# Kernel tuning notes

Hardware: AMD Instinct MI355X
Metric: run time of the kernel (lower is better)

The kernel has to match this reference:

```python
import jax, jax.numpy as jnp
import numpy as np

K = 1.0          # manifold curvature parameter (Lorentz hyperboloid <x,x>_L = -K)
NUM_HEADS = 16
LN_EPS = 1e-5
MID_EPS = 1e-8


def add_time(space):
    # lift a space-like vector onto the hyperboloid: x0 = sqrt(||s||^2 + K)
    t = jnp.sqrt(jnp.sum(space * space, axis=-1, keepdims=True) + K)
    return jnp.concatenate([t, space], axis=-1)


def hlinear(x, W, b):
    # Lorentz linear: dense map on full ambient vector -> space part, recompute time
    return add_time(jnp.einsum('...d,od->...o', x, W) + b)


def hyp_layernorm(x, g, b):
    s = x[..., 1:]
    mu = jnp.mean(s, axis=-1, keepdims=True)
    var = jnp.mean((s - mu) ** 2, axis=-1, keepdims=True)
    s = (s - mu) * jax.lax.rsqrt(var + LN_EPS) * g + b
    return add_time(s)


def hyp_relu(x):
    return add_time(jax.nn.relu(x[..., 1:]))


def lorentz_norm(v):
    # sqrt(|<v,v>_L|) with clamp for numerical safety
    inner = -v[..., 0] ** 2 + jnp.sum(v[..., 1:] ** 2, axis=-1)
    return jnp.sqrt(jnp.maximum(jnp.abs(inner), MID_EPS))


def midpoint_pair(z, x):
    # manifold.midpoint(stack([z, x], dim=-2)).squeeze(): mean then project back
    ave = 0.5 * (z + x)
    return jnp.sqrt(K) * ave / lorentz_norm(ave)[..., None]


def attention(x, Wq, bq, Wk, bk, Wv, bv, Wo, bo):
    B, S, D = x.shape
    dim = D - 1
    H = NUM_HEADS
    dh = dim // H

    def split_heads(t):
        # drop time, split space into heads, re-lift each head onto hyperboloid
        s = t[..., 1:].reshape(B, S, H, dh).transpose(0, 2, 1, 3)  # [B,H,S,dh]
        return add_time(s)                                          # [B,H,S,dh+1]

    qh = split_heads(hlinear(x, Wq, bq))
    kh = split_heads(hlinear(x, Wk, bk))
    vh = split_heads(hlinear(x, Wv, bv))

    # pairwise Lorentz inner product; scores = -d_L^2 / sqrt(dh)
    inner = (jnp.einsum('bhid,bhjd->bhij', qh[..., 1:], kh[..., 1:])
             - qh[..., 0][..., :, None] * kh[..., 0][..., None, :])
    scores = (2.0 / K + 2.0 * inner) / jnp.sqrt(jnp.asarray(dh, x.dtype))
    att = jax.nn.softmax(scores, axis=-1)

    # Lorentz midpoint aggregation of values (weights sum to 1)
    ave = jnp.einsum('bhij,bhjd->bhid', att, vh)
    out = jnp.sqrt(K) * ave / lorentz_norm(ave)[..., None]  # [B,H,S,dh+1]

    # concat head space parts, re-lift, output projection
    out_space = out[..., 1:].transpose(0, 2, 1, 3).reshape(B, S, dim)
    return hlinear(add_time(out_space), Wo, bo)


def reference(x, Wq, bq, Wk, bk, Wv, bv, Wo, bo, ln1_g, ln1_b, W1, c1, W2, c2, ln2_g, ln2_b):
    z = attention(x, Wq, bq, Wk, bk, Wv, bv, Wo, bo)
    x = midpoint_pair(z, x)
    x = hyp_layernorm(x, ln1_g, ln1_b)
    h = hyp_relu(hlinear(x, W1, c1))
    z = hlinear(h, W2, c2)
    x = midpoint_pair(z, x)
    x = hyp_layernorm(x, ln2_g, ln2_b)
    return x


def setup_inputs() -> dict:
    key = jax.random.key(0)
    ks = jax.random.split(key, 12)
    B, S, dim, mlp = 4, 1024, 1024, 4096
    D = dim + 1
    sc = 0.02
    x = add_time(jax.random.normal(ks[0], (B, S, dim), dtype=jnp.float32))
    return {
        'x': x,
        'Wq': sc * jax.random.normal(ks[1], (dim, D), dtype=jnp.float32),
        'bq': jnp.zeros((dim,), jnp.float32),
        'Wk': sc * jax.random.normal(ks[2], (dim, D), dtype=jnp.float32),
        'bk': jnp.zeros((dim,), jnp.float32),
        'Wv': sc * jax.random.normal(ks[3], (dim, D), dtype=jnp.float32),
        'bv': jnp.zeros((dim,), jnp.float32),
        'Wo': sc * jax.random.normal(ks[4], (dim, D), dtype=jnp.float32),
        'bo': jnp.zeros((dim,), jnp.float32),
        'ln1_g': jnp.ones((dim,), jnp.float32),
        'ln1_b': jnp.zeros((dim,), jnp.float32),
        'W1': sc * jax.random.normal(ks[5], (mlp, D), dtype=jnp.float32),
        'c1': jnp.zeros((mlp,), jnp.float32),
        'W2': sc * jax.random.normal(ks[6], (dim, mlp + 1), dtype=jnp.float32),
        'c2': jnp.zeros((dim,), jnp.float32),
        'ln2_g': jnp.ones((dim,), jnp.float32),
        'ln2_b': jnp.zeros((dim,), jnp.float32),
    }
```

## Files before the change

### kernel.cpp

```cpp
#include <hip/hip_runtime.h>

typedef unsigned short u16;
typedef unsigned int   u32;
typedef short bf16x8 __attribute__((ext_vector_type(8)));
typedef float f32x4  __attribute__((ext_vector_type(4)));

#define NTOK 4096
#define SEQ  1024

#define BARRIER() __builtin_amdgcn_s_barrier()
#define VMCNT(n) asm volatile("s_waitcnt vmcnt(" #n ")" ::: "memory")

__device__ __forceinline__ u16 f2bf(float f){
  union { float f; u32 u; } x; x.f = f;
  u32 r = (x.u + 0x7FFFu + ((x.u >> 16) & 1u)) >> 16;
  return (u16)r;
}
__device__ __forceinline__ float bf2f(u16 u){
  union { u32 u; float f; } x; x.u = ((u32)u) << 16; return x.f;
}
__device__ __forceinline__ void gl_lds16(const void* gp, void* lp){
  __builtin_amdgcn_global_load_lds(
      (const __attribute__((address_space(1))) u32*)gp,
      (__attribute__((address_space(3))) u32*)lp, 16, 0, 0);
}

__global__ __launch_bounds__(256) void conv_x(const float* __restrict__ x,
                                              u16* __restrict__ xs, float* __restrict__ xt){
  int t = blockIdx.x * 256 + threadIdx.x;
  int tok = t >> 10, i = t & 1023;
  xs[t] = f2bf(x[(size_t)tok * 1025 + 1 + i]);
  if (i == 0) xt[tok] = x[(size_t)tok * 1025];
}

__global__ __launch_bounds__(256) void conv_w_all(
    const float* __restrict__ Wq, const float* __restrict__ Wk,
    const float* __restrict__ Wv, const float* __restrict__ Wo,
    const float* __restrict__ W1, const float* __restrict__ W2,
    u16* __restrict__ wqkv, u16* __restrict__ wo_s, u16* __restrict__ w1_s, u16* __restrict__ w2_s,
    float* __restrict__ wqkv0, float* __restrict__ wo0, float* __restrict__ w10, float* __restrict__ w20)
{
  int t = blockIdx.x * 256 + threadIdx.x;
  const int M1 = 1 << 20;
  const float* W; u16* Wb; float* w0; int shift; int idx;
  if (t < 4 * M1){
    int region = t >> 20; idx = t & (M1 - 1); shift = 10;
    if (region == 0)      { W = Wq; Wb = wqkv;          w0 = wqkv0; }
    else if (region == 1) { W = Wk; Wb = wqkv + M1;     w0 = wqkv0 + 1024; }
    else if (region == 2) { W = Wv; Wb = wqkv + 2 * M1; w0 = wqkv0 + 2048; }
    else                  { W = Wo; Wb = wo_s;          w0 = wo0; }
  } else if (t < 8 * M1){
    idx = t - 4 * M1; shift = 10; W = W1; Wb = w1_s; w0 = w10;
  } else {
    idx = t - 8 * M1; shift = 12; W = W2; Wb = w2_s; w0 = w20;
  }
  int Kin = 1 << shift;
  int r = idx >> shift, i = idx & (Kin - 1);
  Wb[idx] = f2bf(W[(size_t)r * (Kin + 1) + 1 + i]);
  if (i == 0) w0[r] = W[(size_t)r * (Kin + 1)];
}

__global__ __launch_bounds__(256) void v_transpose(const u16* __restrict__ qkv,
                                                   const float* __restrict__ vtm,
                                                   u16* __restrict__ vT){
  __shared__ u16 tile[64 * 72];
  const int tid = threadIdx.x;
  const int kt = blockIdx.x, bh = blockIdx.y;
  const int b = bh >> 4, h = bh & 15;
  #pragma unroll
  for (int i = 0; i < 2; i++){
    int c = tid * 2 + i;
    int key = c >> 3, fc = c & 7;
    uint4 v = *(const uint4*)(qkv + ((size_t)(b * 1024 + kt * 64 + key)) * 3072 + 2048 + h * 64 + fc * 8);
    *(uint4*)&tile[key * 72 + fc * 8] = v;
  }
  __syncthreads();
  for (int c = tid; c < 520; c += 256){
    int vtr = c >> 3, kc = c & 7;
    union { uint4 v; u16 s[8]; } d;
    if (vtr == 0){
      #pragma unroll
      for (int j = 0; j < 8; j++) d.s[j] = f2bf(vtm[(size_t)bh * 1024 + kt * 64 + kc * 8 + j]);
    } else {
      int f = vtr - 1;
      #pragma unroll
      for (int j = 0; j < 8; j++) d.s[j] = tile[(kc * 8 + j) * 72 + f];
    }
    *(uint4*)(vT + ((size_t)bh * 65 + vtr) * 1024 + kt * 64 + kc * 8) = d.v;
  }
}

__global__ __launch_bounds__(512, 2) void gemm_bt(
    const u16* __restrict__ Ag, int lda, const u16* __restrict__ Bg, int ldb,
    const float* __restrict__ at, int at_mode, const float* __restrict__ b0,
    const float* __restrict__ bias_a, const float* __restrict__ bias_b, const float* __restrict__ bias_c,
    u16* __restrict__ Cbf, int ldc, int Kslice, int mode,
    float* __restrict__ qtv, float* __restrict__ ktv, float* __restrict__ vtm,
    float* __restrict__ rowsq)
{
  __shared__ u16 smem[65536];
  const int tid = threadIdx.x;
  const int w = tid >> 6, l = tid & 63;
  const int l15 = l & 15, q = l >> 4;
  const int wr = w >> 2, wc = w & 3;
  const int gx = gridDim.x;
  const int nwg = gx * gridDim.y;
  const int lin = blockIdx.y * gx + blockIdx.x;
  const int swz = (lin & 7) * (nwg >> 3) + (lin >> 3);
  const int m0 = (swz / gx) * 256, n0 = (swz % gx) * 256;
  const int ks = blockIdx.z;
  const int kbeg = ks * Kslice;

  f32x4 acc[8][4] = {};
  bf16x8 af[4][2], b0f[2][2], b1f[2][2];

  auto stageA = [&](int kt, int buf, int qm){
    #pragma unroll
    for (int ii = 0; ii < 2; ii++){
      int s = (w * 2 + ii) * 64 + l;
      int kk = s >> 9, rem = s & 511;
      int ridx = rem >> 2, cp = rem & 3;
      int kc = (cp - (ridx >> 1)) & 3;
      int trow = ((ridx >> 6) << 7) + qm * 64 + (ridx & 63);
      gl_lds16(Ag + (size_t)(m0 + trow) * lda + kt + kk * 32 + kc * 8,
               &smem[(buf * 2 + qm) * 8192 + (w * 2 + ii) * 512]);
    }
  };
  auto stageB = [&](int kt, int buf, int qn){
    #pragma unroll
    for (int ii = 0; ii < 2; ii++){
      int s = (w * 2 + ii) * 64 + l;
      int kk = s >> 9, rem = s & 511;
      int ridx = rem >> 2, cp = rem & 3;
      int kc = (cp - (ridx >> 1)) & 3;
      int trow = ((ridx >> 5) << 6) + qn * 32 + (ridx & 31);
      gl_lds16(Bg + (size_t)(n0 + trow) * ldb + kt + kk * 32 + kc * 8,
               &smem[32768 + (buf * 2 + qn) * 8192 + (w * 2 + ii) * 512]);
    }
  };
  auto loadA = [&](int buf, int qm){
    #pragma unroll
    for (int i2 = 0; i2 < 4; i2++){
      int ridx = wr * 64 + i2 * 16 + l15;
      int slot = ridx * 4 + ((q + (ridx >> 1)) & 3);
      #pragma unroll
      for (int kk = 0; kk < 2; kk++)
        af[i2][kk] = *(const bf16x8*)&smem[(buf * 2 + qm) * 8192 + kk * 4096 + slot * 8];
    }
  };
  auto loadB = [&](int buf, int qn, bf16x8 (&bb)[2][2]){
    #pragma unroll
    for (int j2 = 0; j2 < 2; j2++){
      int ridx = wc * 32 + j2 * 16 + l15;
      int slot = ridx * 4 + ((q + (ridx >> 1)) & 3);
      #pragma unroll
      for (int kk = 0; kk < 2; kk++)
        bb[j2][kk] = *(const bf16x8*)&smem[32768 + (buf * 2 + qn) * 8192 + kk * 4096 + slot * 8];
    }
  };
  auto mma4 = [&](int qm, int qn, bf16x8 (&bb)[2][2]){
    __builtin_amdgcn_s_setprio(1);
    #pragma unroll
    for (int i2 = 0; i2 < 4; i2++)
      #pragma unroll
      for (int j2 = 0; j2 < 2; j2++)
        #pragma unroll
        for (int kk = 0; kk < 2; kk++)
          acc[qm * 4 + i2][qn * 2 + j2] = __builtin_amdgcn_mfma_f32_16x16x32_bf16(
              af[i2][kk], bb[j2][kk], acc[qm * 4 + i2][qn * 2 + j2], 0, 0, 0);
    __builtin_amdgcn_s_setprio(0);
  };

  stageA(kbeg, 0, 0);
  stageB(kbeg, 0, 0);
  stageB(kbeg, 0, 1);
  stageA(kbeg, 0, 1);
  stageA(kbeg + 64, 1, 0);
  stageB(kbeg + 64, 1, 1);
  stageA(kbeg + 64, 1, 1);
  VMCNT(6);
  BARRIER();

  const int NI = Kslice >> 7;
  for (int it = 0; it < NI; it++){
    const int kb = kbeg + it * 128;
    const bool more = (it + 1 < NI);
    loadA(0, 0); loadB(0, 0, b0f);
    stageB(kb + 64, 1, 0);
    BARRIER(); mma4(0, 0, b0f); BARRIER();
    loadB(0, 1, b1f);
    if (more) stageA(kb + 128, 0, 0);
    BARRIER(); mma4(0, 1, b1f); BARRIER();
    loadA(0, 1);
    if (more) stageB(kb + 128, 0, 1);
    BARRIER(); mma4(1, 1, b1f); BARRIER();
    loadB(0, 0, b0f);
    if (more) stageA(kb + 128, 0, 1);
    if (more) { VMCNT(6); } else { VMCNT(0); }
    BARRIER(); mma4(1, 0, b0f); BARRIER();
    loadA(1, 0); loadB(1, 0, b0f);
    if (more) stageB(kb + 128, 0, 0);
    BARRIER(); mma4(0, 0, b0f); BARRIER();
    loadB(1, 1, b1f);
    if (more) stageA(kb + 192, 1, 0);
    BARRIER(); mma4(0, 1, b1f); BARRIER();
    loadA(1, 1);
    if (more) stageB(kb + 192, 1, 1);
    BARRIER(); mma4(1, 1, b1f); BARRIER();
    loadB(1, 0, b0f);
    if (more) stageA(kb + 192, 1, 1);
    if (more) { VMCNT(6); }
    BARRIER(); mma4(1, 0, b0f); BARRIER();
  }

  const size_t Mtot = (size_t)gridDim.y * 256;
  const size_t slice_off = (size_t)ks * Mtot * ldc;
  #pragma unroll
  for (int ai = 0; ai < 8; ai++){
    const int rb = wr * 128 + (ai >> 2) * 64 + (ai & 3) * 16 + q * 4;
    float atv[4];
    #pragma unroll
    for (int r = 0; r < 4; r++){
      float a = at[m0 + rb + r];
      atv[r] = at_mode ? sqrtf(a + 1.f) : a;
    }
    float p[4] = {0.f, 0.f, 0.f, 0.f};
    #pragma unroll
    for (int bj = 0; bj < 4; bj++){
      const int col = n0 + wc * 64 + (bj >> 1) * 32 + (bj & 1) * 16 + l15;
      float b0v = b0[col];
      float bv;
      if (mode == 0) bv = (col < 1024) ? bias_a[col] : (col < 2048) ? bias_b[col - 1024] : bias_c[col - 2048];
      else bv = bias_a[col];
      #pragma unroll
      for (int r = 0; r < 4; r++){
        size_t row = (size_t)(m0 + rb + r);
        float add = (ks == 0) ? (atv[r] * b0v + bv) : 0.f;
        float v = acc[ai][bj][r] + add;
        if (mode == 2) v = fmaxf(v, 0.f);
        Cbf[slice_off + row * ldc + col] = f2bf(v);
        if (mode != 1) p[r] += v * v;
      }
    }
    if (mode != 1){
      #pragma unroll
      for (int r = 0; r < 4; r++){
        float s = p[r];
        s += __shfl_xor(s, 1, 64); s += __shfl_xor(s, 2, 64);
        s += __shfl_xor(s, 4, 64); s += __shfl_xor(s, 8, 64);
        if (l15 == 0){
          int row = m0 + rb + r;
          if (mode == 2){
            atomicAdd(&rowsq[row], s);
          } else {
            int ch = (n0 + wc * 64) >> 6;
            int bb = row >> 10, sidx = row & 1023;
            float t = sqrtf(s + 1.f);
            if (ch < 16)      qtv[((size_t)bb * 16 + ch) * 1024 + sidx] = t;
            else if (ch < 32) ktv[((size_t)bb * 16 + ch - 16) * 1024 + sidx] = t;
            else              vtm[((size_t)bb * 16 + ch - 32) * 1024 + sidx] = t;
          }
        }
      }
    }
  }
}

__global__ __launch_bounds__(512) void attn_kernel(
    const u16* __restrict__ qkv, const float* __restrict__ qt,
    const float* __restrict__ ktm, const u16* __restrict__ vT,
    u16* __restrict__ aout, float* __restrict__ aot_sq)
{
  __shared__ u16 smem[30720];
  u16* Qlds = smem;
  u16* Kl0 = smem + 8192;
  u16* Kl1 = smem + 12288;
  u16* Vl0 = smem + 16384;
  u16* Vl1 = smem;
  u16* Plds = smem + 21504;
  const int tid = threadIdx.x;
  const int w = tid >> 6, l = tid & 63;
  const int l15 = l & 15, qd = l >> 4;
  const int q0 = blockIdx.x * 128;
  const int bh = blockIdx.y;
  const int b = bh >> 4, h = bh & 15;
  const size_t tokbase = (size_t)b << 10;

  #pragma unroll
  for (int i = 0; i < 2; i++){
    int c = i * 512 + w * 64 + l;
    int row = c >> 3, kc = ((c & 7) - row) & 7;
    gl_lds16(qkv + (tokbase + q0 + row) * 3072 + h * 64 + kc * 8, &Qlds[(i * 512 + w * 64) * 8]);
  }
  __syncthreads();
  bf16x8 aq[2];
  {
    int row = w * 16 + l15;
    #pragma unroll
    for (int kk = 0; kk < 2; kk++)
      aq[kk] = *(const bf16x8*)&Qlds[(row * 8 + ((kk * 4 + qd + row) & 7)) * 8];
  }
  float tq[4];
  #pragma unroll
  for (int r = 0; r < 4; r++)
    tq[r] = qt[(size_t)bh * SEQ + q0 + w * 16 + qd * 4 + r];

  auto stage_kv = [&](int kt, int buf){
    u16* K = buf ? Kl1 : Kl0;
    u16* V = buf ? Vl1 : Vl0;
    int c = w * 64 + l;
    int row = c >> 3, kc = ((c & 7) - row) & 7;
    gl_lds16(qkv + (tokbase + kt * 64 + row) * 3072 + 1024 + h * 64 + kc * 8, &K[w * 512]);
    gl_lds16(vT + ((size_t)bh * 65 + row) * 1024 + kt * 64 + kc * 8, &V[w * 512]);
    if (w == 0 && l < 8)
      gl_lds16(vT + ((size_t)bh * 65 + 64) * 1024 + kt * 64 + (l & 7) * 8, &V[4096]);
  };

  float mrow[4] = {-1e30f, -1e30f, -1e30f, -1e30f};
  f32x4 acco[5] = {};

  stage_kv(0, 0);
  for (int kt = 0; kt < 16; kt++){
    __syncthreads();
    if (kt + 1 < 16) stage_kv(kt + 1, (kt + 1) & 1);
    u16* K = (kt & 1) ? Kl1 : Kl0;
    u16* V = (kt & 1) ? Vl1 : Vl0;

    float sc[4][4];
    float mx[4] = {-1e30f, -1e30f, -1e30f, -1e30f};
    #pragma unroll
    for (int ct = 0; ct < 4; ct++){
      f32x4 z = {0.f, 0.f, 0.f, 0.f};
      int key = ct * 16 + l15;
      #pragma unroll
      for (int kk = 0; kk < 2; kk++){
        bf16x8 bk = *(const bf16x8*)&K[(key * 8 + ((kk * 4 + qd + key) & 7)) * 8];
        z = __builtin_amdgcn_mfma_f32_16x16x32_bf16(aq[kk], bk, z, 0, 0, 0);
      }
      float tk = ktm[(size_t)bh * SEQ + kt * 64 + key];
      #pragma unroll
      for (int r = 0; r < 4; r++){
        float s = 0.25f + 0.25f * (z[r] - tq[r] * tk);
        sc[ct][r] = s;
        mx[r] = fmaxf(mx[r], s);
      }
    }
    #pragma unroll
    for (int r = 0; r < 4; r++){
      #pragma unroll
      for (int msk = 1; msk < 16; msk <<= 1)
        mx[r] = fmaxf(mx[r], __shfl_xor(mx[r], msk, 64));
      float mnew = fmaxf(mrow[r], mx[r]);
      float alpha = __expf(mrow[r] - mnew);
      mrow[r] = mnew;
      #pragma unroll
      for (int co = 0; co < 5; co++) acco[co][r] *= alpha;
      mx[r] = mnew;
    }
    #pragma unroll
    for (int ct = 0; ct < 4; ct++)
      #pragma unroll
      for (int r = 0; r < 4; r++)
        Plds[w * 1152 + (qd * 4 + r) * 72 + ct * 16 + l15] = f2bf(__expf(sc[ct][r] - mx[r]));
    asm volatile("s_waitcnt lgkmcnt(0)" ::: "memory");
    bf16x8 ap[2];
    #pragma unroll
    for (int kk = 0; kk < 2; kk++)
      ap[kk] = *(const bf16x8*)&Plds[w * 1152 + l15 * 72 + kk * 32 + qd * 8];
    #pragma unroll
    for (int co = 0; co < 5; co++){
      int vtr = co * 16 + l15;
      #pragma unroll
      for (int kk = 0; kk < 2; kk++){
        bf16x8 bv = *(const bf16x8*)&V[(vtr * 8 + ((kk * 4 + qd + vtr) & 7)) * 8];
        acco[co] = __builtin_amdgcn_mfma_f32_16x16x32_bf16(ap[kk], bv, acco[co], 0, 0, 0);
      }
    }
  }
  #pragma unroll
  for (int r = 0; r < 4; r++){
    float ss = 0.f;
    #pragma unroll
    for (int co = 0; co < 5; co++){
      int col = co * 16 + l15;
      float v = acco[co][r];
      if (col == 0) ss -= v * v;
      else if (col < 65) ss += v * v;
    }
    #pragma unroll
    for (int msk = 1; msk < 16; msk <<= 1) ss += __shfl_xor(ss, msk, 64);
    float v0b = __shfl(acco[0][r], l & 48, 64);
    float sp = ss + v0b * v0b;
    float rn = rsqrtf(fmaxf(fabsf(ss), 1e-8f));
    size_t rowg = tokbase + q0 + w * 16 + qd * 4 + r;
    if (l15 == 0) atomicAdd(&aot_sq[rowg], sp * rn * rn);
    #pragma unroll
    for (int co = 0; co < 5; co++){
      int col = co * 16 + l15;
      if (col >= 1 && col < 65)
        aout[rowg * 1024 + h * 64 + col - 1] = f2bf(acco[co][r] * rn);
    }
  }
}

__device__ __forceinline__ float block_sum(float v, float* red){
  int tid = threadIdx.x;
  #pragma unroll
  for (int m = 1; m < 64; m <<= 1) v += __shfl_xor(v, m, 64);
  __syncthreads();
  if ((tid & 63) == 0) red[tid >> 6] = v;
  __syncthreads();
  return red[0] + red[1] + red[2] + red[3];
}

__global__ __launch_bounds__(256) void mid_ln(
    const u16* __restrict__ z, const u16* __restrict__ xsb, const float* __restrict__ xtv,
    const float* __restrict__ gam, const float* __restrict__ bet,
    u16* __restrict__ ob, float* __restrict__ ot,
    float* __restrict__ ofull, int mode_out, int nsl)
{
  __shared__ float red[4];
  const int tid = threadIdx.x;
  const int tok = blockIdx.x;
  float zv[4], xv[4], xtime;
  xtime = xtv[tok];
  {
    const u16* xr = xsb + (size_t)tok * 1024;
    #pragma unroll
    for (int j = 0; j < 4; j++) xv[j] = bf2f(xr[tid + j * 256]);
  }
  {
    #pragma unroll
    for (int j = 0; j < 4; j++) zv[j] = 0.f;
    for (int s = 0; s < nsl; s++){
      const u16* zs = z + (size_t)s * NTOK * 1024 + (size_t)tok * 1024;
      #pragma unroll
      for (int j = 0; j < 4; j++) zv[j] += bf2f(zs[tid + j * 256]);
    }
  }
  float ssz = 0.f;
  #pragma unroll
  for (int j = 0; j < 4; j++) ssz += zv[j] * zv[j];
  ssz = block_sum(ssz, red);
  float tz = sqrtf(ssz + 1.f);
  float av[4]; float ssa = 0.f;
  #pragma unroll
  for (int j = 0; j < 4; j++){ av[j] = 0.5f * (zv[j] + xv[j]); ssa += av[j] * av[j]; }
  ssa = block_sum(ssa, red);
  float avt = 0.5f * (tz + xtime);
  float rn = rsqrtf(fmaxf(fabsf(ssa - avt * avt), 1e-8f));
  float uv[4]; float su = 0.f, squ = 0.f;
  #pragma unroll
  for (int j = 0; j < 4; j++){ uv[j] = av[j] * rn; su += uv[j]; squ += uv[j] * uv[j]; }
  su = block_sum(su, red);
  squ = block_sum(squ, red);
  float mu = su * (1.f / 1024.f);
  float var = squ * (1.f / 1024.f) - mu * mu;
  float rv = rsqrtf(fmaxf(var, 0.f) + 1e-5f);
  float sv[4]; float sss = 0.f;
  #pragma unroll
  for (int j = 0; j < 4; j++){
    int i = tid + j * 256;
    sv[j] = (uv[j] - mu) * rv * gam[i] + bet[i];
    sss += sv[j] * sv[j];
  }
  sss = block_sum(sss, red);
  float tout = sqrtf(sss + 1.f);
  if (mode_out == 0){
    #pragma unroll
    for (int j = 0; j < 4; j++){
      int i = tid + j * 256;
      ob[(size_t)tok * 1024 + i] = f2bf(sv[j]);
    }
    if (tid == 0) ot[tok] = tout;
  } else {
    float* orow = ofull + (size_t)tok * 1025;
    #pragma unroll
    for (int j = 0; j < 4; j++) orow[1 + tid + j * 256] = sv[j];
    if (tid == 0) orow[0] = tout;
  }
}

extern "C" void kernel_launch(void* const* d_in, const int* in_sizes, int n_in,
                              void* d_out, int out_size, void* d_ws, size_t ws_size,
                              hipStream_t stream){
  const float* x   = (const float*)d_in[0];
  const float* Wq  = (const float*)d_in[1];
  const float* bq  = (const float*)d_in[2];
  const float* Wk  = (const float*)d_in[3];
  const float* bk  = (const float*)d_in[4];
  const float* Wv  = (const float*)d_in[5];
  const float* bv  = (const float*)d_in[6];
  const float* Wo  = (const float*)d_in[7];
  const float* bo  = (const float*)d_in[8];
  const float* g1  = (const float*)d_in[9];
  const float* be1 = (const float*)d_in[10];
  const float* W1  = (const float*)d_in[11];
  const float* c1  = (const float*)d_in[12];
  const float* W2  = (const float*)d_in[13];
  const float* c2  = (const float*)d_in[14];
  const float* g2  = (const float*)d_in[15];
  const float* be2 = (const float*)d_in[16];
  float* out = (float*)d_out;

  char* p = (char*)d_ws;
  auto take = [&](size_t n){ char* r = p; p += (n + 255) & ~(size_t)255; return r; };
  u16*   xs    = (u16*)  take((size_t)NTOK * 1024 * 2);
  float* xt    = (float*)take(NTOK * 4);
  u16*   wqkv  = (u16*)  take((size_t)3072 * 1024 * 2);
  float* wqkv0 = (float*)take(3072 * 4);
  u16*   wo_s  = (u16*)  take((size_t)1024 * 1024 * 2);
  float* wo0   = (float*)take(1024 * 4);
  u16*   w1_s  = (u16*)  take((size_t)4096 * 1024 * 2);
  float* w10   = (float*)take(4096 * 4);
  u16*   w2_s  = (u16*)  take((size_t)1024 * 4096 * 2);
  float* w20   = (float*)take(1024 * 4);
  u16*   qkvb  = (u16*)  take((size_t)NTOK * 3072 * 2);
  float* qtv   = (float*)take((size_t)64 * 1024 * 4);
  float* ktv   = (float*)take((size_t)64 * 1024 * 4);
  float* vtm   = (float*)take((size_t)64 * 1024 * 4);
  u16*   vT    = (u16*)  take((size_t)64 * 65 * 1024 * 2);
  u16*   aoutb = (u16*)  take((size_t)NTOK * 1024 * 2);
  float* sqbuf = (float*)take((size_t)2 * NTOK * 4);
  float* aot_sq = sqbuf;
  float* htv_sq = sqbuf + NTOK;
  u16*   zbuf  = (u16*)  take((size_t)4 * NTOK * 1024 * 2);
  u16*   x1b   = (u16*)  take((size_t)NTOK * 1024 * 2);
  float* x1t   = (float*)take(NTOK * 4);
  u16*   hbuf  = (u16*)  take((size_t)NTOK * 4096 * 2);

  hipMemsetAsync(sqbuf, 0, (size_t)2 * NTOK * 4, stream);

  conv_x<<<NTOK * 1024 / 256, 256, 0, stream>>>(x, xs, xt);
  conv_w_all<<<(12 * 1024 * 1024) / 256, 256, 0, stream>>>(
      Wq, Wk, Wv, Wo, W1, W2, wqkv, wo_s, w1_s, w2_s, wqkv0, wo0, w10, w20);

  gemm_bt<<<dim3(12, 16), 512, 0, stream>>>(xs, 1024, wqkv, 1024, xt, 0, wqkv0,
      bq, bk, bv, qkvb, 3072, 1024, 0, qtv, ktv, vtm, nullptr);
  v_transpose<<<dim3(16, 64), 512 / 2, 0, stream>>>(qkvb, vtm, vT);
  attn_kernel<<<dim3(8, 64), 512, 0, stream>>>(qkvb, qtv, ktv, vT, aoutb, aot_sq);
  gemm_bt<<<dim3(4, 16, 4), 512, 0, stream>>>(aoutb, 1024, wo_s, 1024, aot_sq, 1, wo0,
      bo, nullptr, nullptr, zbuf, 1024, 256, 1, nullptr, nullptr, nullptr, nullptr);
  mid_ln<<<NTOK, 256, 0, stream>>>(zbuf, xs, xt, g1, be1,
      x1b, x1t, nullptr, 0, 4);
  gemm_bt<<<dim3(16, 16), 512, 0, stream>>>(x1b, 1024, w1_s, 1024, x1t, 0, w10,
      c1, nullptr, nullptr, hbuf, 4096, 1024, 2, nullptr, nullptr, nullptr, htv_sq);
  gemm_bt<<<dim3(4, 16, 4), 512, 0, stream>>>(hbuf, 4096, w2_s, 4096, htv_sq, 1, w20,
      c2, nullptr, nullptr, zbuf, 1024, 1024, 1, nullptr, nullptr, nullptr, nullptr);
  mid_ln<<<NTOK, 256, 0, stream>>>(zbuf, x1b, x1t, g2, be2,
      nullptr, nullptr, out, 1, 4);
}
```

Baseline: 413.7 us.

## Add 128x128 GEMM kernel for QKV/out/W2 projections and raise MFMA priority in attention

Introduces a new 256-thread GEMM kernel with 128x128 tiles and double-buffered LDS staging. The QKV, output-projection and W2 GEMMs now use it, with more blocks and split-K reduced from 4 to 2, which halves the partial sums mid_ln has to combine. The 256-tile kernel is kept only for W1 and has its epilogue trimmed. The attention kernel wraps its MFMA sections in s_setprio so matrix work gets issued first. The aim is better CU occupancy and load balance on the narrower GEMMs, at the cost of less data reuse per tile.

```diff
diff --git a/kernel.cpp b/kernel.cpp
--- a/kernel.cpp
+++ b/kernel.cpp
@@ -90,12 +90,128 @@
   }
 }
 
-__global__ __launch_bounds__(512, 2) void gemm_bt(
-    const u16* __restrict__ Ag, int lda, const u16* __restrict__ Bg, int ldb,
+__global__ __launch_bounds__(256) void gemm128(
+    const u16* __restrict__ A, int lda, const u16* __restrict__ Bm, int ldb,
     const float* __restrict__ at, int at_mode, const float* __restrict__ b0,
     const float* __restrict__ bias_a, const float* __restrict__ bias_b, const float* __restrict__ bias_c,
     u16* __restrict__ Cbf, int ldc, int Kslice, int mode,
     float* __restrict__ qtv, float* __restrict__ ktv, float* __restrict__ vtm,
+    float* __restrict__ rowsq)
+{
+  __shared__ u16 As[2][128 * 64];
+  __shared__ u16 Bs[2][128 * 64];
+  const int tid = threadIdx.x;
+  const int w = tid >> 6, l = tid & 63;
+  const int l15 = l & 15, q = l >> 4;
+  const int m0 = blockIdx.y * 128, n0 = blockIdx.x * 128;
+  const int ks = blockIdx.z;
+  const int kbeg = ks * Kslice;
+  const int kend = kbeg + Kslice;
+  const int wr = w >> 1, wc = w & 1;
+  f32x4 acc[4][4] = {};
+
+  auto stage = [&](int kt, int buf){
+    #pragma unroll
+    for (int half = 0; half < 2; half++){
+      #pragma unroll
+      for (int i = 0; i < 2; i++){
+        int s = (w * 2 + i) * 64 + l;
+        int row = s >> 2;
+        int kc = ((s & 3) - (s >> 3)) & 3;
+        gl_lds16(A  + (size_t)(m0 + row) * lda + kt + half * 32 + kc * 8,
+                 &As[buf][half * 4096 + (w * 2 + i) * 512]);
+        gl_lds16(Bm + (size_t)(n0 + row) * ldb + kt + half * 32 + kc * 8,
+                 &Bs[buf][half * 4096 + (w * 2 + i) * 512]);
+      }
+    }
+  };
+  auto compute = [&](int buf, int half){
+    bf16x8 af[4], bfr[4];
+    #pragma unroll
+    for (int i = 0; i < 4; i++){
+      int row = wr * 64 + i * 16 + l15;
+      int slot = row * 4 + ((q + (row >> 1)) & 3);
+      af[i] = *(const bf16x8*)&As[buf][half * 4096 + slot * 8];
+    }
+    #pragma unroll
+    for (int j = 0; j < 4; j++){
+      int row = wc * 64 + j * 16 + l15;
+      int slot = row * 4 + ((q + (row >> 1)) & 3);
+      bfr[j] = *(const bf16x8*)&Bs[buf][half * 4096 + slot * 8];
+    }
+    #pragma unroll
+    for (int i = 0; i < 4; i++)
+      #pragma unroll
+      for (int j = 0; j < 4; j++)
+        acc[i][j] = __builtin_amdgcn_mfma_f32_16x16x32_bf16(af[i], bfr[j], acc[i][j], 0, 0, 0);
+  };
+
+  stage(kbeg, 0);
+  for (int kt = kbeg; kt < kend; kt += 128){
+    __syncthreads();
+    if (kt + 64 < kend) stage(kt + 64, 1);
+    compute(0, 0); compute(0, 1);
+    __syncthreads();
+    if (kt + 128 < kend) stage(kt + 128, 0);
+    compute(1, 0); compute(1, 1);
+  }
+
+  const size_t slice_off = (size_t)ks * (size_t)(gridDim.y * 128) * ldc;
+  #pragma unroll
+  for (int i = 0; i < 4; i++){
+    float atv[4];
+    #pragma unroll
+    for (int r = 0; r < 4; r++){
+      float a = at[m0 + wr * 64 + i * 16 + q * 4 + r];
+      atv[r] = at_mode ? sqrtf(a + 1.f) : a;
+    }
+    float p[4] = {0.f, 0.f, 0.f, 0.f};
+    #pragma unroll
+    for (int j = 0; j < 4; j++){
+      int col = n0 + wc * 64 + j * 16 + l15;
+      float b0v = b0[col];
+      float bv;
+      if (mode == 0) bv = (col < 1024) ? bias_a[col] : (col < 2048) ? bias_b[col - 1024] : bias_c[col - 2048];
+      else bv = bias_a[col];
+      #pragma unroll
+      for (int r = 0; r < 4; r++){
+        size_t row = (size_t)(m0 + wr * 64 + i * 16 + q * 4 + r);
+        float add = (ks == 0) ? (atv[r] * b0v + bv) : 0.f;
+        float v = acc[i][j][r] + add;
+        if (mode == 2) v = fmaxf(v, 0.f);
+        Cbf[slice_off + row * ldc + col] = f2bf(v);
+        if (mode != 1) p[r] += v * v;
+      }
+    }
+    if (mode != 1){
+      #pragma unroll
+      for (int r = 0; r < 4; r++){
+        float s = p[r];
+        s += __shfl_xor(s, 1, 64); s += __shfl_xor(s, 2, 64);
+        s += __shfl_xor(s, 4, 64); s += __shfl_xor(s, 8, 64);
+        if (l15 == 0){
+          int row = m0 + wr * 64 + i * 16 + q * 4 + r;
+          if (mode == 2){
+            atomicAdd(&rowsq[row], s);
+          } else {
+            int ch = (n0 + wc * 64) >> 6;
+            int bb = row >> 10, sidx = row & 1023;
+            float t = sqrtf(s + 1.f);
+            if (ch < 16)      qtv[((size_t)bb * 16 + ch) * 1024 + sidx] = t;
+            else if (ch < 32) ktv[((size_t)bb * 16 + ch - 16) * 1024 + sidx] = t;
+            else              vtm[((size_t)bb * 16 + ch - 32) * 1024 + sidx] = t;
+          }
+        }
+      }
+    }
+  }
+}
+
+__global__ __launch_bounds__(512, 2) void gemm256(
+    const u16* __restrict__ Ag, int lda, const u16* __restrict__ Bg, int ldb,
+    const float* __restrict__ at, int at_mode, const float* __restrict__ b0,
+    const float* __restrict__ bias_a,
+    u16* __restrict__ Cbf, int ldc, int Kslice, int mode,
     float* __restrict__ rowsq)
 {
   __shared__ u16 smem[65536];
@@ -229,9 +345,7 @@
     for (int bj = 0; bj < 4; bj++){
       const int col = n0 + wc * 64 + (bj >> 1) * 32 + (bj & 1) * 16 + l15;
       float b0v = b0[col];
-      float bv;
-      if (mode == 0) bv = (col < 1024) ? bias_a[col] : (col < 2048) ? bias_b[col - 1024] : bias_c[col - 2048];
-      else bv = bias_a[col];
+      float bv = bias_a[col];
       #pragma unroll
       for (int r = 0; r < 4; r++){
         size_t row = (size_t)(m0 + rb + r);
@@ -248,19 +362,7 @@
         float s = p[r];
         s += __shfl_xor(s, 1, 64); s += __shfl_xor(s, 2, 64);
         s += __shfl_xor(s, 4, 64); s += __shfl_xor(s, 8, 64);
-        if (l15 == 0){
-          int row = m0 + rb + r;
-          if (mode == 2){
-            atomicAdd(&rowsq[row], s);
-          } else {
-            int ch = (n0 + wc * 64) >> 6;
-            int bb = row >> 10, sidx = row & 1023;
-            float t = sqrtf(s + 1.f);
-            if (ch < 16)      qtv[((size_t)bb * 16 + ch) * 1024 + sidx] = t;
-            else if (ch < 32) ktv[((size_t)bb * 16 + ch - 16) * 1024 + sidx] = t;
-            else              vtm[((size_t)bb * 16 + ch - 32) * 1024 + sidx] = t;
-          }
-        }
+        if (l15 == 0) atomicAdd(&rowsq[m0 + rb + r], s);
       }
     }
   }
@@ -332,11 +434,13 @@
     for (int ct = 0; ct < 4; ct++){
       f32x4 z = {0.f, 0.f, 0.f, 0.f};
       int key = ct * 16 + l15;
+      __builtin_amdgcn_s_setprio(1);
       #pragma unroll
       for (int kk = 0; kk < 2; kk++){
         bf16x8 bk = *(const bf16x8*)&K[(key * 8 + ((kk * 4 + qd + key) & 7)) * 8];
         z = __builtin_amdgcn_mfma_f32_16x16x32_bf16(aq[kk], bk, z, 0, 0, 0);
       }
+      __builtin_amdgcn_s_setprio(0);
       float tk = ktm[(size_t)bh * SEQ + kt * 64 + key];
       #pragma unroll
       for (int r = 0; r < 4; r++){
@@ -367,6 +471,7 @@
     #pragma unroll
     for (int kk = 0; kk < 2; kk++)
       ap[kk] = *(const bf16x8*)&Plds[w * 1152 + l15 * 72 + kk * 32 + qd * 8];
+    __builtin_amdgcn_s_setprio(1);
     #pragma unroll
     for (int co = 0; co < 5; co++){
       int vtr = co * 16 + l15;
@@ -376,6 +481,7 @@
         acco[co] = __builtin_amdgcn_mfma_f32_16x16x32_bf16(ap[kk], bv, acco[co], 0, 0, 0);
       }
     }
+    __builtin_amdgcn_s_setprio(0);
   }
   #pragma unroll
   for (int r = 0; r < 4; r++){
@@ -535,18 +641,18 @@
   conv_w_all<<<(12 * 1024 * 1024) / 256, 256, 0, stream>>>(
       Wq, Wk, Wv, Wo, W1, W2, wqkv, wo_s, w1_s, w2_s, wqkv0, wo0, w10, w20);
 
-  gemm_bt<<<dim3(12, 16), 512, 0, stream>>>(xs, 1024, wqkv, 1024, xt, 0, wqkv0,
+  gemm128<<<dim3(24, 32), 256, 0, stream>>>(xs, 1024, wqkv, 1024, xt, 0, wqkv0,
       bq, bk, bv, qkvb, 3072, 1024, 0, qtv, ktv, vtm, nullptr);
-  v_transpose<<<dim3(16, 64), 512 / 2, 0, stream>>>(qkvb, vtm, vT);
+  v_transpose<<<dim3(16, 64), 256, 0, stream>>>(qkvb, vtm, vT);
   attn_kernel<<<dim3(8, 64), 512, 0, stream>>>(qkvb, qtv, ktv, vT, aoutb, aot_sq);
-  gemm_bt<<<dim3(4, 16, 4), 512, 0, stream>>>(aoutb, 1024, wo_s, 1024, aot_sq, 1, wo0,
-      bo, nullptr, nullptr, zbuf, 1024, 256, 1, nullptr, nullptr, nullptr, nullptr);
+  gemm128<<<dim3(8, 32, 2), 256, 0, stream>>>(aoutb, 1024, wo_s, 1024, aot_sq, 1, wo0,
+      bo, nullptr, nullptr, zbuf, 1024, 512, 1, nullptr, nullptr, nullptr, nullptr);
   mid_ln<<<NTOK, 256, 0, stream>>>(zbuf, xs, xt, g1, be1,
-      x1b, x1t, nullptr, 0, 4);
-  gemm_bt<<<dim3(16, 16), 512, 0, stream>>>(x1b, 1024, w1_s, 1024, x1t, 0, w10,
-      c1, nullptr, nullptr, hbuf, 4096, 1024, 2, nullptr, nullptr, nullptr, htv_sq);
-  gemm_bt<<<dim3(4, 16, 4), 512, 0, stream>>>(hbuf, 4096, w2_s, 4096, htv_sq, 1, w20,
-      c2, nullptr, nullptr, zbuf, 1024, 1024, 1, nullptr, nullptr, nullptr, nullptr);
+      x1b, x1t, nullptr, 0, 2);
+  gemm256<<<dim3(16, 16), 512, 0, stream>>>(x1b, 1024, w1_s, 1024, x1t, 0, w10,
+      c1, hbuf, 4096, 1024, 2, htv_sq);
+  gemm128<<<dim3(8, 32, 2), 256, 0, stream>>>(hbuf, 4096, w2_s, 4096, htv_sq, 1, w20,
+      c2, nullptr, nullptr, zbuf, 1024, 2048, 1, nullptr, nullptr, nullptr, nullptr);
   mid_ln<<<NTOK, 256, 0, stream>>>(zbuf, x1b, x1t, g2, be2,
-      nullptr, nullptr, out, 1, 4);
-}
+      nullptr, nullptr, out, 1, 2);
+}
```

After: 407.4 us. Within noise of the previous version (-1.5%).
